# Optimization experiments

Measured on AMD Instinct MI355X. Metric: run time of the kernel, lower is better.

## Reference

```python
import jax, jax.numpy as jnp
import numpy as np

EPS = 1e-7  # tf.keras.backend.epsilon()
DEGREE = 5
SCALE_BASE = 1.0
SCALE_LEGENDRE = 1.0


def legendre_basis(x, degree):
    # min/max normalization over the feature axis -> x_norm in [-1, 1]
    x_min = jnp.min(x, axis=-1, keepdims=True)
    x_max = jnp.max(x, axis=-1, keepdims=True)
    x_norm = 2.0 * (x - x_min) / (x_max - x_min + EPS) - 1.0
    polys = [jnp.ones_like(x_norm), x_norm]
    for n in range(2, degree + 1):
        p_n = ((2 * n - 1) * x_norm * polys[-1] - (n - 1) * polys[-2]) / n
        polys.append(p_n)
    return jnp.stack(polys, axis=-1)  # [b, i, degree+1]


def setup_inputs() -> dict:
    key = jax.random.key(0)
    k1, k2, k3 = jax.random.split(key, 3)
    b, i, o, d = 4096, 1024, 1024, DEGREE + 1
    x = jax.random.normal(k1, (b, i), dtype=jnp.float32)
    # HeUniform: limit = sqrt(6 / fan_in)
    lim_b = np.sqrt(6.0 / i)
    base_weight = jax.random.uniform(k2, (i, o), dtype=jnp.float32, minval=-lim_b, maxval=lim_b)
    legendre_weight = jax.random.uniform(k3, (i, o, d), dtype=jnp.float32, minval=-lim_b, maxval=lim_b)
    return {"x": x, "base_weight": base_weight, "legendre_weight": legendre_weight}


def reference(x, base_weight, legendre_weight):
    base_output = jax.nn.silu(x @ base_weight)  # [b, o]
    basis = legendre_basis(x, DEGREE)  # [b, i, d]
    # 'bi,iod,bid->bo' == fold x into the basis then contract (i, d)
    xb = x[..., None] * basis  # [b, i, d]
    legendre_output = jnp.einsum('bid,iod->bo', xb, legendre_weight)
    return SCALE_BASE * base_output + SCALE_LEGENDRE * legendre_output
```

## Files before the change

kernel.cpp:

```cpp
#include <hip/hip_runtime.h>
#include <stdint.h>

typedef unsigned short u16;
typedef unsigned int   u32;
typedef __attribute__((ext_vector_type(8)))  short bhalf8;
typedef __attribute__((ext_vector_type(16))) float f32x16;

#define B_ROWS 4096
#define I_DIM  1024
#define O_DIM  1024
#define N_D    6
#define K_LEG  (I_DIM * N_D)

#define BM 256
#define BN 256
#define BK 32
#define NU 56
#define SLOT_BYTES 32768
#define LDS_BYTES  131072

__device__ __forceinline__ u16 f2b(float f) {
  u32 u = __float_as_uint(f);
  return (u16)((u + 0x7fffu + ((u >> 16) & 1u)) >> 16);
}
__device__ __forceinline__ float b2f(u16 h) {
  return __uint_as_float((u32)h << 16);
}

__device__ __forceinline__ void gld_lds16(const void* g, void* l) {
  __builtin_amdgcn_global_load_lds(
      (const __attribute__((address_space(1))) u32*)(uintptr_t)g,
      (__attribute__((address_space(3))) u32*)(u32)(uintptr_t)l, 16, 0, 0);
}

#define RS 201
__global__ void k_prep(const float* __restrict__ bw, const float* __restrict__ lw,
                       const float* __restrict__ x,
                       u16* __restrict__ Bb, u16* __restrict__ Bl,
                       u16* __restrict__ Ab, u16* __restrict__ Al) {
  __shared__ float t[32 * RS];
  if (blockIdx.x < 1024) {
    const int bx = blockIdx.x & 31, by = blockIdx.x >> 5;
    const int i0 = by * 32, o0 = bx * 32;
    const int c = threadIdx.x & 31, r0 = threadIdx.x >> 5;
    #pragma unroll
    for (int k = 0; k < 4; ++k) {
      int r = r0 + k * 8;
      t[r * 33 + c] = bw[(size_t)(i0 + r) * O_DIM + o0 + c];
    }
    __syncthreads();
    #pragma unroll
    for (int k = 0; k < 4; ++k) {
      int r = r0 + k * 8;
      Bb[(size_t)(o0 + r) * I_DIM + i0 + c] = f2b(t[c * 33 + r]);
    }
  } else if (blockIdx.x < 2048) {
    const int blk = blockIdx.x - 1024;
    const int bx = blk & 31, by = blk >> 5;
    const int i0 = by * 32, o0 = bx * 32;
    for (int q = threadIdx.x; q < 32 * 48; q += 256) {
      int ri = q / 48, s4 = q % 48;
      float4 v = *(const float4*)(lw + (size_t)(i0 + ri) * (O_DIM * N_D) + o0 * N_D + s4 * 4);
      float* p = t + ri * RS + s4 * 4;
      p[0] = v.x; p[1] = v.y; p[2] = v.z; p[3] = v.w;
    }
    __syncthreads();
    for (int q = threadIdx.x; q < 32 * 96; q += 256) {
      int ro = q / 96, k = q % 96;
      int e0 = 2 * k, e1 = 2 * k + 1;
      float v0 = t[(e0 / 6) * RS + ro * 6 + (e0 % 6)];
      float v1 = t[(e1 / 6) * RS + ro * 6 + (e1 % 6)];
      u32* dst = (u32*)(Bl + (size_t)(o0 + ro) * K_LEG + i0 * N_D);
      dst[k] = (u32)f2b(v0) | ((u32)f2b(v1) << 16);
    }
  } else {
    const int b = blockIdx.x - 2048;
    const int tt = threadIdx.x;
    float4 v = ((const float4*)(x + (size_t)b * I_DIM))[tt];
    float mn = fminf(fminf(v.x, v.y), fminf(v.z, v.w));
    float mx = fmaxf(fmaxf(v.x, v.y), fmaxf(v.z, v.w));
    #pragma unroll
    for (int off = 32; off > 0; off >>= 1) {
      mn = fminf(mn, __shfl_xor(mn, off, 64));
      mx = fmaxf(mx, __shfl_xor(mx, off, 64));
    }
    __shared__ float smn[4], smx[4];
    if ((tt & 63) == 0) { smn[tt >> 6] = mn; smx[tt >> 6] = mx; }
    __syncthreads();
    mn = fminf(fminf(smn[0], smn[1]), fminf(smn[2], smn[3]));
    mx = fmaxf(fmaxf(smx[0], smx[1]), fmaxf(smx[2], smx[3]));
    float sc = 2.0f / (mx - mn + 1e-7f);

    float xs[4] = {v.x, v.y, v.z, v.w};
    u32 lb[12];
    #pragma unroll
    for (int e = 0; e < 4; ++e) {
      float xv = xs[e];
      float xn = (xv - mn) * sc - 1.0f;
      float p0 = 1.0f, p1 = xn;
      float p2 = (3.0f * xn * p1 - 1.0f * p0) * (1.0f / 2.0f);
      float p3 = (5.0f * xn * p2 - 2.0f * p1) * (1.0f / 3.0f);
      float p4 = (7.0f * xn * p3 - 3.0f * p2) * (1.0f / 4.0f);
      float p5 = (9.0f * xn * p4 - 4.0f * p3) * (1.0f / 5.0f);
      lb[e * 3 + 0] = (u32)f2b(xv * p0) | ((u32)f2b(xv * p1) << 16);
      lb[e * 3 + 1] = (u32)f2b(xv * p2) | ((u32)f2b(xv * p3) << 16);
      lb[e * 3 + 2] = (u32)f2b(xv * p4) | ((u32)f2b(xv * p5) << 16);
    }
    u32 a0 = (u32)f2b(xs[0]) | ((u32)f2b(xs[1]) << 16);
    u32 a1 = (u32)f2b(xs[2]) | ((u32)f2b(xs[3]) << 16);
    *(uint2*)(Ab + (size_t)b * I_DIM + tt * 4) = make_uint2(a0, a1);
    uint4* dl = (uint4*)(Al + (size_t)b * K_LEG + tt * 24);
    dl[0] = make_uint4(lb[0], lb[1], lb[2], lb[3]);
    dl[1] = make_uint4(lb[4], lb[5], lb[6], lb[7]);
    dl[2] = make_uint4(lb[8], lb[9], lb[10], lb[11]);
  }
}

__global__ __launch_bounds__(512, 2) void k_gemm(
    const u16* __restrict__ Ab, const u16* __restrict__ Bb,
    const u16* __restrict__ Al, const u16* __restrict__ Bl,
    u16* __restrict__ Pb) {
  extern __shared__ char lds[];

  const int tid  = threadIdx.x;
  const int wave = tid >> 6;
  const int lane = tid & 63;
  const int wm = wave >> 2;
  const int wn = wave & 3;
  const u32 lr = (u32)lane & 31;
  const u32 hi = (u32)lane >> 5;

  const int bid   = blockIdx.x;
  const int by    = bid >> 6;
  const int p_    = bid & 63;
  const int bx    = p_ >> 2;
  const int split = p_ & 3;
  const size_t brow = (size_t)bx * BM;
  const size_t bcol = (size_t)by * BN;
  const bool s0 = (split == 0);
  const int legbase = s0 ? 0 : (24 + 56 * (split - 1));

  const int r4 = tid >> 2;
  const u32 skey = (((u32)r4 >> 1) & 3) ^ (((u32)r4 >> 3) & 3);
  const size_t cs = (size_t)(((u32)(tid & 3) ^ skey) * 8);
  char* const l0 = lds + (u32)wave * 1024;

  const u16 *gA0, *gA1, *gB0, *gB1;
  auto set_ptrs = [&](const u16* A, const u16* Bt, size_t ldk, size_t kt) {
    const size_t ko = kt * BK + cs;
    gA0 = A  + (brow + r4) * ldk + ko;
    gA1 = A  + (brow + 128 + r4) * ldk + ko;
    gB0 = Bt + (bcol + r4) * ldk + ko;
    gB1 = Bt + (bcol + 128 + r4) * ldk + ko;
  };
  if (s0) set_ptrs(Ab, Bb, I_DIM, 0);
  else    set_ptrs(Al, Bl, K_LEG, (size_t)legbase);

  auto stage = [&](int v) {
    if (s0 && v == 32) set_ptrs(Al, Bl, K_LEG, 0);
    char* d = l0 + (size_t)(v & 3) * SLOT_BYTES;
    gld_lds16(gA0, d);          gld_lds16(gA1, d + 8192);
    gld_lds16(gB0, d + 16384);  gld_lds16(gB1, d + 24576);
    gA0 += BK; gA1 += BK; gB0 += BK; gB1 += BK;
  };

  const u32 key = ((lr >> 1) & 3) ^ ((lr >> 3) & 3);
  const u32 c00 = ((0 + hi) ^ key) * 16;
  const u32 c10 = ((2 + hi) ^ key) * 16;
  const u32 abase_r = (u32)wm * 8192 + lr * 64;
  const u32 bbase_r = 16384u + ((u32)wn >> 1) * 8192 + ((u32)wn & 1) * 4096 + lr * 64;

  f32x16 acc[4][2] = {};
  bhalf8 a0[4], b0[2], a1[4], b1[2], a2[4], b2[2];

  auto silu = [&]() {
    #pragma unroll
    for (int m = 0; m < 4; ++m)
      #pragma unroll
      for (int n = 0; n < 2; ++n)
        #pragma unroll
        for (int j = 0; j < 16; ++j) {
          float v = acc[m][n][j];
          acc[m][n][j] = v / (1.0f + __expf(-v));
        }
  };

#define FILL(u1, CH, AA, BB) do {                                             \
    const char* pn_ = lds + (size_t)((u1) & 3) * SLOT_BYTES;                  \
    BB[0] = *(const bhalf8*)(pn_ + bbase_r + (CH));                           \
    BB[1] = *(const bhalf8*)(pn_ + bbase_r + 2048 + (CH));                    \
    AA[0] = *(const bhalf8*)(pn_ + abase_r + (CH));                           \
    AA[1] = *(const bhalf8*)(pn_ + abase_r + 2048 + (CH));                    \
    AA[2] = *(const bhalf8*)(pn_ + abase_r + 4096 + (CH));                    \
    AA[3] = *(const bhalf8*)(pn_ + abase_r + 6144 + (CH));                    \
  } while (0)

#define MM(AA, BB) do {                                                       \
    __builtin_amdgcn_sched_barrier(0);                                        \
    __builtin_amdgcn_s_setprio(1);                                            \
    _Pragma("unroll")                                                         \
    for (int m = 0; m < 4; ++m)                                               \
      _Pragma("unroll")                                                       \
      for (int n = 0; n < 2; ++n)                                             \
        acc[m][n] = __builtin_amdgcn_mfma_f32_32x32x16_bf16(AA[m], BB[n], acc[m][n], 0, 0, 0); \
    __builtin_amdgcn_s_setprio(0);                                            \
    __builtin_amdgcn_sched_barrier(0);                                        \
  } while (0)

#define TILE(u, PA, PB, QA, QB, RA, RB) do {                                  \
    const int u_ = (u);                                                       \
    if (s0 && u_ == 32) silu();                                               \
    if (u_ <= NU - 3) {                                                       \
      stage(u_ + 2);                                                          \
      asm volatile("s_waitcnt vmcnt(4)" ::: "memory");   \
    } else {                                                                  \
      asm volatile("s_waitcnt vmcnt(0)" ::: "memory");                        \
    }                                                                         \
    __builtin_amdgcn_s_barrier();                                             \
    if (u_ < NU - 1) FILL(u_ + 1, c00, RA, RB);                               \
    MM(PA, PB);                                                               \
    if (u_ < NU - 1) FILL(u_ + 1, c10, PA, PB);                               \
    MM(QA, QB);                                                               \
  } while (0)

  stage(0); stage(1);
  asm volatile("s_waitcnt vmcnt(4)" ::: "memory");
  __builtin_amdgcn_s_barrier();
  FILL(0, c00, a0, b0);
  FILL(0, c10, a1, b1);

  for (int t = 0; t < 18; ++t) {
    const int u = t * 3;
    TILE(u,     a0, b0, a1, b1, a2, b2);
    TILE(u + 1, a2, b2, a0, b0, a1, b1);
    TILE(u + 2, a1, b1, a2, b2, a0, b0);
  }
  TILE(54, a0, b0, a1, b1, a2, b2);
  TILE(55, a2, b2, a0, b0, a1, b1);
#undef TILE
#undef MM
#undef FILL

  u16* dst = Pb + (size_t)split * ((size_t)B_ROWS * O_DIM);
  #pragma unroll
  for (int m = 0; m < 4; ++m)
    #pragma unroll
    for (int n = 0; n < 2; ++n) {
      const size_t rb = brow + wm * 128 + m * 32 + 4 * hi;
      const size_t c  = bcol + wn * 64 + n * 32 + lr;
      #pragma unroll
      for (int j = 0; j < 16; ++j) {
        const size_t r = rb + (j & 3) + 8 * (j >> 2);
        dst[r * O_DIM + c] = f2b(acc[m][n][j]);
      }
    }
}

__global__ void k_reduce(float* __restrict__ out, const u16* __restrict__ Pb) {
  const size_t i = (size_t)blockIdx.x * 256 + threadIdx.x;
  const size_t NE = (size_t)B_ROWS * O_DIM;
  ushort4 p0 = ((const ushort4*)Pb)[i];
  ushort4 p1 = ((const ushort4*)(Pb + NE))[i];
  ushort4 p2 = ((const ushort4*)(Pb + 2 * NE))[i];
  ushort4 p3 = ((const ushort4*)(Pb + 3 * NE))[i];
  float4 a;
  a.x = b2f(p0.x) + b2f(p1.x) + b2f(p2.x) + b2f(p3.x);
  a.y = b2f(p0.y) + b2f(p1.y) + b2f(p2.y) + b2f(p3.y);
  a.z = b2f(p0.z) + b2f(p1.z) + b2f(p2.z) + b2f(p3.z);
  a.w = b2f(p0.w) + b2f(p1.w) + b2f(p2.w) + b2f(p3.w);
  ((float4*)out)[i] = a;
}

extern "C" void kernel_launch(void* const* d_in, const int* in_sizes, int n_in,
                              void* d_out, int out_size, void* d_ws, size_t ws_size,
                              hipStream_t stream) {
  const float* x  = (const float*)d_in[0];
  const float* bw = (const float*)d_in[1];
  const float* lw = (const float*)d_in[2];
  float* out = (float*)d_out;

  char* w = (char*)d_ws;
  u16* Ab = (u16*)(w);
  u16* Al = (u16*)(w + (size_t)8   * 1024 * 1024);
  u16* Bb = (u16*)(w + (size_t)56  * 1024 * 1024);
  u16* Bl = (u16*)(w + (size_t)58  * 1024 * 1024);
  u16* Pb = (u16*)(w + (size_t)72  * 1024 * 1024);

  hipFuncSetAttribute((const void*)k_gemm,
                      hipFuncAttributeMaxDynamicSharedMemorySize, LDS_BYTES);

  k_prep  <<<dim3(2048 + B_ROWS), 256, 0, stream>>>(bw, lw, x, Bb, Bl, Ab, Al);
  k_gemm  <<<dim3(256), 512, LDS_BYTES, stream>>>(Ab, Bb, Al, Bl, Pb);
  k_reduce<<<dim3((B_ROWS * O_DIM / 4) / 256), 256, 0, stream>>>(out, Pb);
}
```

Before: 101.2 us.

## Fuse prep, GEMM and reduce into one cooperative kernel with grid syncs

```diff
diff --git a/kernel.cpp b/kernel.cpp
--- a/kernel.cpp
+++ b/kernel.cpp
@@ -1,5 +1,8 @@
 #include <hip/hip_runtime.h>
+#include <hip/hip_cooperative_groups.h>
 #include <stdint.h>
+
+namespace cg = cooperative_groups;
 
 typedef unsigned short u16;
 typedef unsigned int   u32;
@@ -33,96 +36,81 @@
       (__attribute__((address_space(3))) u32*)(u32)(uintptr_t)l, 16, 0, 0);
 }
 
-#define RS 201
-__global__ void k_prep(const float* __restrict__ bw, const float* __restrict__ lw,
-                       const float* __restrict__ x,
-                       u16* __restrict__ Bb, u16* __restrict__ Bl,
-                       u16* __restrict__ Ab, u16* __restrict__ Al) {
-  __shared__ float t[32 * RS];
-  if (blockIdx.x < 1024) {
-    const int bx = blockIdx.x & 31, by = blockIdx.x >> 5;
-    const int i0 = by * 32, o0 = bx * 32;
-    const int c = threadIdx.x & 31, r0 = threadIdx.x >> 5;
-    #pragma unroll
-    for (int k = 0; k < 4; ++k) {
-      int r = r0 + k * 8;
-      t[r * 33 + c] = bw[(size_t)(i0 + r) * O_DIM + o0 + c];
-    }
-    __syncthreads();
-    #pragma unroll
-    for (int k = 0; k < 4; ++k) {
-      int r = r0 + k * 8;
-      Bb[(size_t)(o0 + r) * I_DIM + i0 + c] = f2b(t[c * 33 + r]);
-    }
-  } else if (blockIdx.x < 2048) {
-    const int blk = blockIdx.x - 1024;
-    const int bx = blk & 31, by = blk >> 5;
-    const int i0 = by * 32, o0 = bx * 32;
-    for (int q = threadIdx.x; q < 32 * 48; q += 256) {
-      int ri = q / 48, s4 = q % 48;
-      float4 v = *(const float4*)(lw + (size_t)(i0 + ri) * (O_DIM * N_D) + o0 * N_D + s4 * 4);
-      float* p = t + ri * RS + s4 * 4;
-      p[0] = v.x; p[1] = v.y; p[2] = v.z; p[3] = v.w;
-    }
-    __syncthreads();
-    for (int q = threadIdx.x; q < 32 * 96; q += 256) {
-      int ro = q / 96, k = q % 96;
-      int e0 = 2 * k, e1 = 2 * k + 1;
-      float v0 = t[(e0 / 6) * RS + ro * 6 + (e0 % 6)];
-      float v1 = t[(e1 / 6) * RS + ro * 6 + (e1 % 6)];
-      u32* dst = (u32*)(Bl + (size_t)(o0 + ro) * K_LEG + i0 * N_D);
-      dst[k] = (u32)f2b(v0) | ((u32)f2b(v1) << 16);
-    }
-  } else {
-    const int b = blockIdx.x - 2048;
-    const int tt = threadIdx.x;
-    float4 v = ((const float4*)(x + (size_t)b * I_DIM))[tt];
-    float mn = fminf(fminf(v.x, v.y), fminf(v.z, v.w));
-    float mx = fmaxf(fmaxf(v.x, v.y), fmaxf(v.z, v.w));
-    #pragma unroll
-    for (int off = 32; off > 0; off >>= 1) {
-      mn = fminf(mn, __shfl_xor(mn, off, 64));
-      mx = fmaxf(mx, __shfl_xor(mx, off, 64));
-    }
-    __shared__ float smn[4], smx[4];
-    if ((tt & 63) == 0) { smn[tt >> 6] = mn; smx[tt >> 6] = mx; }
-    __syncthreads();
-    mn = fminf(fminf(smn[0], smn[1]), fminf(smn[2], smn[3]));
-    mx = fmaxf(fmaxf(smx[0], smx[1]), fmaxf(smx[2], smx[3]));
-    float sc = 2.0f / (mx - mn + 1e-7f);
-
-    float xs[4] = {v.x, v.y, v.z, v.w};
-    u32 lb[12];
-    #pragma unroll
-    for (int e = 0; e < 4; ++e) {
-      float xv = xs[e];
-      float xn = (xv - mn) * sc - 1.0f;
-      float p0 = 1.0f, p1 = xn;
-      float p2 = (3.0f * xn * p1 - 1.0f * p0) * (1.0f / 2.0f);
-      float p3 = (5.0f * xn * p2 - 2.0f * p1) * (1.0f / 3.0f);
-      float p4 = (7.0f * xn * p3 - 3.0f * p2) * (1.0f / 4.0f);
-      float p5 = (9.0f * xn * p4 - 4.0f * p3) * (1.0f / 5.0f);
-      lb[e * 3 + 0] = (u32)f2b(xv * p0) | ((u32)f2b(xv * p1) << 16);
-      lb[e * 3 + 1] = (u32)f2b(xv * p2) | ((u32)f2b(xv * p3) << 16);
-      lb[e * 3 + 2] = (u32)f2b(xv * p4) | ((u32)f2b(xv * p5) << 16);
-    }
-    u32 a0 = (u32)f2b(xs[0]) | ((u32)f2b(xs[1]) << 16);
-    u32 a1 = (u32)f2b(xs[2]) | ((u32)f2b(xs[3]) << 16);
-    *(uint2*)(Ab + (size_t)b * I_DIM + tt * 4) = make_uint2(a0, a1);
-    uint4* dl = (uint4*)(Al + (size_t)b * K_LEG + tt * 24);
-    dl[0] = make_uint4(lb[0], lb[1], lb[2], lb[3]);
-    dl[1] = make_uint4(lb[4], lb[5], lb[6], lb[7]);
-    dl[2] = make_uint4(lb[8], lb[9], lb[10], lb[11]);
+__global__ __launch_bounds__(512, 2) void k_fused(
+    const float* __restrict__ bw, const float* __restrict__ lw,
+    const float* __restrict__ x,
+    u16* __restrict__ Ab, u16* __restrict__ Al,
+    u16* __restrict__ Bb, u16* __restrict__ Bl,
+    u16* __restrict__ Pb, float* __restrict__ out) {
+  extern __shared__ char lds[];
+
+  const int tid = threadIdx.x;
+  const int bid = blockIdx.x;
+  cg::grid_group grid = cg::this_grid();
+
+  {
+    const int gid = bid * 512 + tid;
+
+    for (int j = gid; j < O_DIM * I_DIM; j += 131072) {
+      const int o = j >> 10, i = j & 1023;
+      Bb[j] = f2b(bw[(size_t)i * O_DIM + o]);
+    }
+    for (int j = gid; j < O_DIM * I_DIM; j += 131072) {
+      const int o = j >> 10, i = j & 1023;
+      const float* s = lw + ((size_t)i * O_DIM + o) * N_D;
+      float2 a = *(const float2*)(s);
+      float2 b = *(const float2*)(s + 2);
+      float2 c = *(const float2*)(s + 4);
+      u32* d = (u32*)(Bl + (size_t)o * K_LEG + (size_t)i * N_D);
+      d[0] = (u32)f2b(a.x) | ((u32)f2b(a.y) << 16);
+      d[1] = (u32)f2b(b.x) | ((u32)f2b(b.y) << 16);
+      d[2] = (u32)f2b(c.x) | ((u32)f2b(c.y) << 16);
+    }
+    float* smn = (float*)lds;
+    float* smx = smn + 8;
+    for (int r = bid; r < B_ROWS; r += 256) {
+      float2 v = ((const float2*)(x + (size_t)r * I_DIM))[tid];
+      float mn = fminf(v.x, v.y);
+      float mx = fmaxf(v.x, v.y);
+      #pragma unroll
+      for (int off = 32; off > 0; off >>= 1) {
+        mn = fminf(mn, __shfl_xor(mn, off, 64));
+        mx = fmaxf(mx, __shfl_xor(mx, off, 64));
+      }
+      if ((tid & 63) == 0) { smn[tid >> 6] = mn; smx[tid >> 6] = mx; }
+      __syncthreads();
+      mn = smn[0]; mx = smx[0];
+      #pragma unroll
+      for (int w = 1; w < 8; ++w) { mn = fminf(mn, smn[w]); mx = fmaxf(mx, smx[w]); }
+      const float sc = 2.0f / (mx - mn + 1e-7f);
+
+      float xs[2] = {v.x, v.y};
+      u32 lb[6];
+      #pragma unroll
+      for (int e = 0; e < 2; ++e) {
+        const float xv = xs[e];
+        const float xn = (xv - mn) * sc - 1.0f;
+        const float p0 = 1.0f, p1 = xn;
+        const float p2 = (3.0f * xn * p1 - 1.0f * p0) * (1.0f / 2.0f);
+        const float p3 = (5.0f * xn * p2 - 2.0f * p1) * (1.0f / 3.0f);
+        const float p4 = (7.0f * xn * p3 - 3.0f * p2) * (1.0f / 4.0f);
+        const float p5 = (9.0f * xn * p4 - 4.0f * p3) * (1.0f / 5.0f);
+        lb[e * 3 + 0] = (u32)f2b(xv * p0) | ((u32)f2b(xv * p1) << 16);
+        lb[e * 3 + 1] = (u32)f2b(xv * p2) | ((u32)f2b(xv * p3) << 16);
+        lb[e * 3 + 2] = (u32)f2b(xv * p4) | ((u32)f2b(xv * p5) << 16);
+      }
+      ((u32*)(Ab + (size_t)r * I_DIM))[tid] =
+          (u32)f2b(xs[0]) | ((u32)f2b(xs[1]) << 16);
+      uint2* dl = (uint2*)(Al + (size_t)r * K_LEG + (size_t)tid * 12);
+      dl[0] = make_uint2(lb[0], lb[1]);
+      dl[1] = make_uint2(lb[2], lb[3]);
+      dl[2] = make_uint2(lb[4], lb[5]);
+      __syncthreads();
+    }
   }
-}
-
-__global__ __launch_bounds__(512, 2) void k_gemm(
-    const u16* __restrict__ Ab, const u16* __restrict__ Bb,
-    const u16* __restrict__ Al, const u16* __restrict__ Bl,
-    u16* __restrict__ Pb) {
-  extern __shared__ char lds[];
-
-  const int tid  = threadIdx.x;
+
+  grid.sync();
+
   const int wave = tid >> 6;
   const int lane = tid & 63;
   const int wm = wave >> 2;
@@ -130,7 +118,6 @@
   const u32 lr = (u32)lane & 31;
   const u32 hi = (u32)lane >> 5;
 
-  const int bid   = blockIdx.x;
   const int by    = bid >> 6;
   const int p_    = bid & 63;
   const int bx    = p_ >> 2;
@@ -140,50 +127,51 @@
   const bool s0 = (split == 0);
   const int legbase = s0 ? 0 : (24 + 56 * (split - 1));
 
-  const int r4 = tid >> 2;
-  const u32 skey = (((u32)r4 >> 1) & 3) ^ (((u32)r4 >> 3) & 3);
-  const size_t cs = (size_t)(((u32)(tid & 3) ^ skey) * 8);
-  char* const l0 = lds + (u32)wave * 1024;
-
-  const u16 *gA0, *gA1, *gB0, *gB1;
-  auto set_ptrs = [&](const u16* A, const u16* Bt, size_t ldk, size_t kt) {
-    const size_t ko = kt * BK + cs;
-    gA0 = A  + (brow + r4) * ldk + ko;
-    gA1 = A  + (brow + 128 + r4) * ldk + ko;
-    gB0 = Bt + (bcol + r4) * ldk + ko;
-    gB1 = Bt + (bcol + 128 + r4) * ldk + ko;
-  };
-  if (s0) set_ptrs(Ab, Bb, I_DIM, 0);
-  else    set_ptrs(Al, Bl, K_LEG, (size_t)legbase);
-
-  auto stage = [&](int v) {
-    if (s0 && v == 32) set_ptrs(Al, Bl, K_LEG, 0);
-    char* d = l0 + (size_t)(v & 3) * SLOT_BYTES;
-    gld_lds16(gA0, d);          gld_lds16(gA1, d + 8192);
-    gld_lds16(gB0, d + 16384);  gld_lds16(gB1, d + 24576);
-    gA0 += BK; gA1 += BK; gB0 += BK; gB1 += BK;
-  };
-
-  const u32 key = ((lr >> 1) & 3) ^ ((lr >> 3) & 3);
-  const u32 c00 = ((0 + hi) ^ key) * 16;
-  const u32 c10 = ((2 + hi) ^ key) * 16;
-  const u32 abase_r = (u32)wm * 8192 + lr * 64;
-  const u32 bbase_r = 16384u + ((u32)wn >> 1) * 8192 + ((u32)wn & 1) * 4096 + lr * 64;
-
-  f32x16 acc[4][2] = {};
-  bhalf8 a0[4], b0[2], a1[4], b1[2], a2[4], b2[2];
-
-  auto silu = [&]() {
-    #pragma unroll
-    for (int m = 0; m < 4; ++m)
-      #pragma unroll
-      for (int n = 0; n < 2; ++n)
+  {
+    const int r4 = tid >> 2;
+    const u32 skey = (((u32)r4 >> 1) & 3) ^ (((u32)r4 >> 3) & 3);
+    const size_t cs = (size_t)(((u32)(tid & 3) ^ skey) * 8);
+    char* const l0 = lds + (u32)wave * 1024;
+
+    const u16 *gA0, *gA1, *gB0, *gB1;
+    auto set_ptrs = [&](const u16* A, const u16* Bt, size_t ldk, size_t kt) {
+      const size_t ko = kt * BK + cs;
+      gA0 = A  + (brow + r4) * ldk + ko;
+      gA1 = A  + (brow + 128 + r4) * ldk + ko;
+      gB0 = Bt + (bcol + r4) * ldk + ko;
+      gB1 = Bt + (bcol + 128 + r4) * ldk + ko;
+    };
+    if (s0) set_ptrs(Ab, Bb, I_DIM, 0);
+    else    set_ptrs(Al, Bl, K_LEG, (size_t)legbase);
+
+    auto stage = [&](int v) {
+      if (s0 && v == 32) set_ptrs(Al, Bl, K_LEG, 0);
+      char* d = l0 + (size_t)(v & 3) * SLOT_BYTES;
+      gld_lds16(gA0, d);          gld_lds16(gA1, d + 8192);
+      gld_lds16(gB0, d + 16384);  gld_lds16(gB1, d + 24576);
+      gA0 += BK; gA1 += BK; gB0 += BK; gB1 += BK;
+    };
+
+    const u32 key = ((lr >> 1) & 3) ^ ((lr >> 3) & 3);
+    const u32 c00 = ((0 + hi) ^ key) * 16;
+    const u32 c10 = ((2 + hi) ^ key) * 16;
+    const u32 abase_r = (u32)wm * 8192 + lr * 64;
+    const u32 bbase_r = 16384u + ((u32)wn >> 1) * 8192 + ((u32)wn & 1) * 4096 + lr * 64;
+
+    f32x16 acc[4][2] = {};
+    bhalf8 a0[4], b0[2], a1[4], b1[2], a2[4], b2[2];
+
+    auto silu = [&]() {
+      #pragma unroll
+      for (int m = 0; m < 4; ++m)
         #pragma unroll
-        for (int j = 0; j < 16; ++j) {
-          float v = acc[m][n][j];
-          acc[m][n][j] = v / (1.0f + __expf(-v));
-        }
-  };
+        for (int n = 0; n < 2; ++n)
+          #pragma unroll
+          for (int j = 0; j < 16; ++j) {
+            float v = acc[m][n][j];
+            acc[m][n][j] = v / (1.0f + __expf(-v));
+          }
+    };
 
 #define FILL(u1, CH, AA, BB) do {                                             \
     const char* pn_ = lds + (size_t)((u1) & 3) * SLOT_BYTES;                  \
@@ -207,7 +195,7 @@
     __builtin_amdgcn_sched_barrier(0);                                        \
   } while (0)
 
-#define TILE(u, PA, PB, QA, QB, RA, RB) do {                                  \
+#define TILE(u, PA, PB_, QA, QB, RA, RB) do {                                 \
     const int u_ = (u);                                                       \
     if (s0 && u_ == 32) silu();                                               \
     if (u_ <= NU - 3) {                                                       \
@@ -218,57 +206,75 @@
     }                                                                         \
     __builtin_amdgcn_s_barrier();                                             \
     if (u_ < NU - 1) FILL(u_ + 1, c00, RA, RB);                               \
-    MM(PA, PB);                                                               \
-    if (u_ < NU - 1) FILL(u_ + 1, c10, PA, PB);                               \
+    MM(PA, PB_);                                                              \
+    if (u_ < NU - 1) FILL(u_ + 1, c10, PA, PB_);                              \
     MM(QA, QB);                                                               \
   } while (0)
 
-  stage(0); stage(1);
-  asm volatile("s_waitcnt vmcnt(4)" ::: "memory");
-  __builtin_amdgcn_s_barrier();
-  FILL(0, c00, a0, b0);
-  FILL(0, c10, a1, b1);
-
-  for (int t = 0; t < 18; ++t) {
-    const int u = t * 3;
-    TILE(u,     a0, b0, a1, b1, a2, b2);
-    TILE(u + 1, a2, b2, a0, b0, a1, b1);
-    TILE(u + 2, a1, b1, a2, b2, a0, b0);
-  }
-  TILE(54, a0, b0, a1, b1, a2, b2);
-  TILE(55, a2, b2, a0, b0, a1, b1);
+    __syncthreads();
+    stage(0); stage(1);
+    asm volatile("s_waitcnt vmcnt(4)" ::: "memory");
+    __builtin_amdgcn_s_barrier();
+    FILL(0, c00, a0, b0);
+    FILL(0, c10, a1, b1);
+
+    for (int t = 0; t < 18; ++t) {
+      const int u = t * 3;
+      TILE(u,     a0, b0, a1, b1, a2, b2);
+      TILE(u + 1, a2, b2, a0, b0, a1, b1);
+      TILE(u + 2, a1, b1, a2, b2, a0, b0);
+    }
+    TILE(54, a0, b0, a1, b1, a2, b2);
+    TILE(55, a2, b2, a0, b0, a1, b1);
 #undef TILE
 #undef MM
 #undef FILL
 
-  u16* dst = Pb + (size_t)split * ((size_t)B_ROWS * O_DIM);
-  #pragma unroll
-  for (int m = 0; m < 4; ++m)
+    u16* dst = Pb + (size_t)split * ((size_t)B_ROWS * O_DIM);
     #pragma unroll
-    for (int n = 0; n < 2; ++n) {
-      const size_t rb = brow + wm * 128 + m * 32 + 4 * hi;
-      const size_t c  = bcol + wn * 64 + n * 32 + lr;
-      #pragma unroll
-      for (int j = 0; j < 16; ++j) {
-        const size_t r = rb + (j & 3) + 8 * (j >> 2);
-        dst[r * O_DIM + c] = f2b(acc[m][n][j]);
+    for (int m = 0; m < 4; ++m)
+      #pragma unroll
+      for (int n = 0; n < 2; ++n) {
+        const size_t rb = brow + wm * 128 + m * 32 + 4 * hi;
+        const size_t c  = bcol + wn * 64 + n * 32 + lr;
+        #pragma unroll
+        for (int j = 0; j < 16; ++j) {
+          const size_t r = rb + (j & 3) + 8 * (j >> 2);
+          dst[r * O_DIM + c] = f2b(acc[m][n][j]);
+        }
       }
-    }
-}
-
-__global__ void k_reduce(float* __restrict__ out, const u16* __restrict__ Pb) {
-  const size_t i = (size_t)blockIdx.x * 256 + threadIdx.x;
-  const size_t NE = (size_t)B_ROWS * O_DIM;
-  ushort4 p0 = ((const ushort4*)Pb)[i];
-  ushort4 p1 = ((const ushort4*)(Pb + NE))[i];
-  ushort4 p2 = ((const ushort4*)(Pb + 2 * NE))[i];
-  ushort4 p3 = ((const ushort4*)(Pb + 3 * NE))[i];
-  float4 a;
-  a.x = b2f(p0.x) + b2f(p1.x) + b2f(p2.x) + b2f(p3.x);
-  a.y = b2f(p0.y) + b2f(p1.y) + b2f(p2.y) + b2f(p3.y);
-  a.z = b2f(p0.z) + b2f(p1.z) + b2f(p2.z) + b2f(p3.z);
-  a.w = b2f(p0.w) + b2f(p1.w) + b2f(p2.w) + b2f(p3.w);
-  ((float4*)out)[i] = a;
+  }
+
+  grid.sync();
+
+  {
+    const size_t NE = (size_t)B_ROWS * O_DIM;
+    const size_t r0 = brow + (size_t)split * 64;
+    for (int q = tid; q < 64 * 256 / 8; q += 512) {
+      const int rl = q >> 5;
+      const int c8 = (q & 31) << 3;
+      const size_t off = (r0 + rl) * O_DIM + bcol + c8;
+      ushort4 a0 = *(const ushort4*)(Pb + off);
+      ushort4 a1 = *(const ushort4*)(Pb + off + 4);
+      ushort4 b0 = *(const ushort4*)(Pb + NE + off);
+      ushort4 b1 = *(const ushort4*)(Pb + NE + off + 4);
+      ushort4 c0 = *(const ushort4*)(Pb + 2 * NE + off);
+      ushort4 c1 = *(const ushort4*)(Pb + 2 * NE + off + 4);
+      ushort4 d0 = *(const ushort4*)(Pb + 3 * NE + off);
+      ushort4 d1 = *(const ushort4*)(Pb + 3 * NE + off + 4);
+      float4 f0, f1;
+      f0.x = b2f(a0.x) + b2f(b0.x) + b2f(c0.x) + b2f(d0.x);
+      f0.y = b2f(a0.y) + b2f(b0.y) + b2f(c0.y) + b2f(d0.y);
+      f0.z = b2f(a0.z) + b2f(b0.z) + b2f(c0.z) + b2f(d0.z);
+      f0.w = b2f(a0.w) + b2f(b0.w) + b2f(c0.w) + b2f(d0.w);
+      f1.x = b2f(a1.x) + b2f(b1.x) + b2f(c1.x) + b2f(d1.x);
+      f1.y = b2f(a1.y) + b2f(b1.y) + b2f(c1.y) + b2f(d1.y);
+      f1.z = b2f(a1.z) + b2f(b1.z) + b2f(c1.z) + b2f(d1.z);
+      f1.w = b2f(a1.w) + b2f(b1.w) + b2f(c1.w) + b2f(d1.w);
+      *(float4*)(out + off)     = f0;
+      *(float4*)(out + off + 4) = f1;
+    }
+  }
 }
 
 extern "C" void kernel_launch(void* const* d_in, const int* in_sizes, int n_in,
@@ -286,10 +292,12 @@
   u16* Bl = (u16*)(w + (size_t)58  * 1024 * 1024);
   u16* Pb = (u16*)(w + (size_t)72  * 1024 * 1024);
 
-  hipFuncSetAttribute((const void*)k_gemm,
+  hipFuncSetAttribute((const void*)k_fused,
                       hipFuncAttributeMaxDynamicSharedMemorySize, LDS_BYTES);
 
-  k_prep  <<<dim3(2048 + B_ROWS), 256, 0, stream>>>(bw, lw, x, Bb, Bl, Ab, Al);
-  k_gemm  <<<dim3(256), 512, LDS_BYTES, stream>>>(Ab, Bb, Al, Bl, Pb);
-  k_reduce<<<dim3((B_ROWS * O_DIM / 4) / 256), 256, 0, stream>>>(out, Pb);
-}
+  void* args[] = { (void*)&bw, (void*)&lw, (void*)&x,
+                   (void*)&Ab, (void*)&Al, (void*)&Bb, (void*)&Bl,
+                   (void*)&Pb, (void*)&out };
+  hipLaunchCooperativeKernel((const void*)k_fused, dim3(256), dim3(512),
+                             args, LDS_BYTES, stream);
+}
```

Result: slower. 196.4 us (+94.1%).
